# Kernel tuning notes

Measured on AMD Instinct MI355X. Metric: run time of the kernel, lower is better.

Reference implementation:

```python
import jax, jax.numpy as jnp
from jax import lax
import numpy as np

B, C, O, NF, H, W = 4, 64, 64, 64, 128, 128
DK = 3
K = DK * DK
PAD = DK // 2


def setup_inputs() -> dict:
    key = jax.random.key(0)
    k0, k1, k2, k3 = jax.random.split(key, 4)
    inputs = jax.random.normal(k0, (B, C, H, W), jnp.float32)
    feat = jax.random.normal(k1, (B, NF, H, W), jnp.float32)
    # small offset-conv weights keep learned offsets in a realistic sub-pixel range
    om_w = jax.random.normal(k2, (C * 3 * K, NF, 3, 3), jnp.float32) * 0.02
    om_b = jnp.zeros((C * 3 * K,), jnp.float32)
    dc_w = jax.random.normal(k3, (O, C, DK, DK), jnp.float32) * (1.0 / np.sqrt(C * K))
    dc_b = jnp.zeros((O,), jnp.float32)
    return dict(inputs=inputs, feat=feat, om_w=om_w, om_b=om_b, dc_w=dc_w, dc_b=dc_b)


def _gather(img, y, x):
    # img: [B,C,H,W]; y,x: int32 [B,C,K,H,W]; zero outside bounds
    valid = (y >= 0) & (y < H) & (x >= 0) & (x < W)
    yc = jnp.clip(y, 0, H - 1)
    xc = jnp.clip(x, 0, W - 1)
    idx = (yc * W + xc).reshape(B, C, K, H * W)
    flat = img.reshape(B, C, 1, H * W)
    v = jnp.take_along_axis(flat, idx, axis=3).reshape(B, C, K, H, W)
    return jnp.where(valid, v, 0.0)


def _forward(inputs, feat, om_w, om_b, dc_w, dc_b):
    # offset/mask conv: nf -> in_nc*3*K, 3x3, pad 1
    off_msk = lax.conv_general_dilated(
        feat, om_w, (1, 1), ((1, 1), (1, 1)),
        dimension_numbers=('NCHW', 'OIHW', 'NCHW')) + om_b[None, :, None, None]
    # offsets interleaved (y,x) per kernel tap per deformable group (= channel)
    off = off_msk[:, :C * 2 * K].reshape(B, C, K, 2, H, W)
    msk = jax.nn.sigmoid(off_msk[:, C * 2 * K:]).reshape(B, C, K, H, W)

    ky = (jnp.arange(K) // DK - PAD).astype(jnp.float32)  # [K]
    kx = (jnp.arange(K) % DK - PAD).astype(jnp.float32)
    hg = jnp.arange(H, dtype=jnp.float32)
    wg = jnp.arange(W, dtype=jnp.float32)
    py = hg[None, None, None, :, None] + ky[None, None, :, None, None] + off[:, :, :, 0]  # [B,C,K,H,W]
    px = wg[None, None, None, None, :] + kx[None, None, :, None, None] + off[:, :, :, 1]

    y0f = jnp.floor(py); x0f = jnp.floor(px)
    wy = py - y0f; wx = px - x0f
    y0 = y0f.astype(jnp.int32); x0 = x0f.astype(jnp.int32)
    y1 = y0 + 1; x1 = x0 + 1

    v00 = _gather(inputs, y0, x0)
    v01 = _gather(inputs, y0, x1)
    v10 = _gather(inputs, y1, x0)
    v11 = _gather(inputs, y1, x1)
    sampled = ((1 - wy) * (1 - wx) * v00 + (1 - wy) * wx * v01
               + wy * (1 - wx) * v10 + wy * wx * v11) * msk  # [B,C,K,H,W]

    out = jnp.einsum('bckhw,ock->bohw', sampled, dc_w.reshape(O, C, K))
    out = out + dc_b[None, :, None, None]
    return jax.nn.relu(out)


def reference(inputs, feat, om_w, om_b, dc_w, dc_b):
    return _forward(inputs, feat, om_w, om_b, dc_w, dc_b)
```

## Files before the change

### kernel.cpp

```cpp
#include <hip/hip_runtime.h>
#include <hip/hip_bf16.h>

typedef __bf16 bf16;
typedef __bf16 bf16x8 __attribute__((ext_vector_type(8)));
typedef __bf16 bf16x4 __attribute__((ext_vector_type(4)));
typedef float f32x4 __attribute__((ext_vector_type(4)));
typedef int i32x4 __attribute__((ext_vector_type(4)));

#define MFMA16(a, b, c) __builtin_amdgcn_mfma_f32_16x16x32_bf16((a), (b), (c), 0, 0, 0)

static constexpr size_t FEATS_OFF = 0;
static constexpr size_t OMW3_OFF  = 8388608;
static constexpr size_t OMB_OFF   = OMW3_OFF + 1990656;
static constexpr size_t DCW_OFF   = OMB_OFF + 6912;
static constexpr size_t PAD_OFF   = DCW_OFF + 73728;


__global__ void prep_featS(const float* __restrict__ feat, bf16* __restrict__ featS) {
    const int hh = blockIdx.x, b = blockIdx.y;
    __shared__ float t[64][129];
    for (int i = threadIdx.x; i < 64 * 32; i += 256) {
        int cf = i >> 5, q = i & 31;
        const float* src = feat + ((size_t)(b * 64 + cf) * 128 + hh) * 128 + q * 4;
        t[cf][q * 4 + 0] = src[0];
        t[cf][q * 4 + 1] = src[1];
        t[cf][q * 4 + 2] = src[2];
        t[cf][q * 4 + 3] = src[3];
    }
    __syncthreads();
    for (int i = threadIdx.x; i < 1024; i += 256) {
        int px = i >> 3, cfb = i & 7;
        int sb = cfb ^ (px & 7);
        bf16x8 v;
#pragma unroll
        for (int e = 0; e < 8; ++e) v[e] = (bf16)t[cfb * 8 + e][px];
        *(bf16x8*)(featS + ((size_t)((b * 128 + hh) * 128 + px) << 6) + sb * 8) = v;
    }
}

__global__ void prep_omw3(const float* __restrict__ om_w, bf16* __restrict__ out) {
    int i = blockIdx.x * 256 + threadIdx.x;
    if (i >= 995328) return;
    int e = i & 511, lane = e >> 3, j = e & 7;
    int q = i >> 9;
    int t = q % 3, q2 = q / 3, kk = q2 % 18, ct = q2 / 18;
    int ck = ct * 16 + (lane & 15);
    int kcol = kk * 32 + (lane >> 4) * 8 + j;
    int tap = kcol >> 6, cf = kcol & 63;
    int ch = (t < 2) ? (ck * 2 + t) : (1152 + ck);
    out[i] = (bf16)om_w[ch * 576 + cf * 9 + tap];
}

__global__ void prep_dcw2p(const float* __restrict__ dc_w, const float* __restrict__ om_b,
                           bf16* __restrict__ dcw2p, float* __restrict__ ombr) {
    int i = blockIdx.x * 256 + threadIdx.x;
    if (i < 36864) {
        int j = i & 7, lane = (i >> 3) & 63, ot = (i >> 9) & 3, win = i >> 11;
        int o = ot * 16 + (lane & 15);
        int ck = win * 32 + (lane >> 4) * 8 + j;
        dcw2p[i] = (bf16)dc_w[o * 576 + ck];
    }
    if (i < 1728) {
        int t = i / 576, ck = i - t * 576;
        int ch = (t < 2) ? (ck * 2 + t) : (1152 + ck);
        ombr[i] = om_b[ch];
    }
}

__global__ void prep_pad(const float* __restrict__ inputs, float* __restrict__ pad) {
    int yy = blockIdx.x, bc = blockIdx.y, xx = threadIdx.x;
    if (xx >= 134) return;
    float v = 0.f;
    if (yy >= 3 && yy <= 130 && xx >= 3 && xx <= 130)
        v = inputs[(size_t)bc * 16384 + (yy - 3) * 128 + (xx - 3)];
    pad[((size_t)bc * 134 + yy) * 134 + xx] = v;
}


__global__ void __launch_bounds__(256, 4)
deform_fused(const float* __restrict__ pad,
             const bf16* __restrict__ featS,
             const bf16* __restrict__ omw3,
             const float* __restrict__ ombr,
             const bf16* __restrict__ dcw2p,
             const float* __restrict__ dcb,
             float* __restrict__ out)
{
    const int bid = blockIdx.x;
    const int P0 = (bid & 1) << 6;
    const int h = (bid >> 1) & 127;
    const int b = bid >> 8;
    const int tid = threadIdx.x;
    const int lane = tid & 63, wid = tid >> 6;
    const int l15 = lane & 15, g = lane >> 4;

    __shared__ __align__(16) unsigned char smem[25344 + 8192];
    char* featB = (char*)smem;
    char* sampB = (char*)smem + 25344;

    for (int i = tid; i < 6336; i += 256) ((unsigned*)featB)[i] = 0u;
    __syncthreads();
    {
        const int s0 = (P0 == 0) ? 0 : 63;
        const int q0 = (P0 == 0) ? 1 : 0;
        for (int i = tid; i < 1560; i += 256) {
            int ky = i / 520, rem = i - ky * 520, row = rem >> 3, c = rem & 7;
            int hh = h - 1 + ky;
            if ((unsigned)hh < 128u) {
                const char* src = (const char*)featS
                    + (((size_t)(b * 128 + hh) * 128 + s0 + row) << 7) + c * 16;
                *(i32x4*)(featB + ((ky * 66 + q0 + row) << 7) + c * 16) = *(const i32x4*)src;
            }
        }
    }
    __syncthreads();

    f32x4 acc2[4];
#pragma unroll
    for (int u = 0; u < 4; ++u) acc2[u] = (f32x4){0.f, 0.f, 0.f, 0.f};

    const float* padb0 = pad + (size_t)b * 64 * 17956;
    const float fx0 = (float)(P0 + l15);

#pragma unroll 1
    for (int blk = 0; blk < 9; ++blk) {
        f32x4 acc1[3][4];
#pragma unroll
        for (int t = 0; t < 3; ++t)
#pragma unroll
            for (int nf = 0; nf < 4; ++nf) acc1[t][nf] = (f32x4){0.f, 0.f, 0.f, 0.f};

        const int ct = blk * 4 + wid;

#pragma unroll 2
        for (int kk = 0; kk < 18; ++kk) {
            const int tap = kk >> 1;
            const int kyp = tap / 3, kxp = tap - 3 * kyp;
            bf16x8 a0 = *(const bf16x8*)(omw3 + (size_t)(((ct * 18 + kk) * 3 + 0) * 512) + lane * 8);
            bf16x8 a1 = *(const bf16x8*)(omw3 + (size_t)(((ct * 18 + kk) * 3 + 1) * 512) + lane * 8);
            bf16x8 a2 = *(const bf16x8*)(omw3 + (size_t)(((ct * 18 + kk) * 3 + 2) * 512) + lane * 8);
            const int q = l15 + kxp;
            const int base = (kyp * 66 + q) * 128 + ((((kk & 1) * 4 + g) ^ ((q + 7) & 7)) << 4);
            bf16x8 bfr[4];
#pragma unroll
            for (int nf = 0; nf < 4; ++nf)
                bfr[nf] = *(const bf16x8*)(featB + base + nf * 2048);
            __builtin_amdgcn_s_setprio(1);
#pragma unroll
            for (int nf = 0; nf < 4; ++nf) {
                acc1[0][nf] = MFMA16(a0, bfr[nf], acc1[0][nf]);
                acc1[1][nf] = MFMA16(a1, bfr[nf], acc1[1][nf]);
                acc1[2][nf] = MFMA16(a2, bfr[nf], acc1[2][nf]);
            }
            __builtin_amdgcn_s_setprio(0);
        }

        bf16x8 aK0 = *(const bf16x8*)(dcw2p + (size_t)(((blk * 2 + 0) * 4 + wid) * 512) + lane * 8);
        bf16x8 aK1 = *(const bf16x8*)(dcw2p + (size_t)(((blk * 2 + 1) * 4 + wid) * 512) + lane * 8);

        {
            unsigned coff[4];
            float bye3[4], bxe3[4], bm[4];
#pragma unroll
            for (int r = 0; r < 4; ++r) {
                int ck = blk * 64 + wid * 16 + g * 4 + r;
                int c = ck / 9, kd = ck - 9 * c, kq = kd / 3;
                coff[r] = (unsigned)(c * 17956);
                bye3[r] = ombr[ck] + (float)(h + kq + 2);
                bxe3[r] = ombr[576 + ck] + (float)(kd - 3 * kq + 2);
                bm[r]   = ombr[1152 + ck];
            }
#pragma unroll
            for (int nf = 0; nf < 4; ++nf) {
                const float fxn = fx0 + 16.f * (float)nf;
                float s[4];
#pragma unroll
                for (int r = 0; r < 4; ++r) {
                    float py3 = acc1[0][nf][r] + bye3[r];
                    float px3 = acc1[1][nf][r] + bxe3[r] + fxn;
                    float lg  = acc1[2][nf][r] + bm[r];
                    py3 = fminf(fmaxf(py3, 0.5f), 132.5f);
                    px3 = fminf(fmaxf(px3, 0.5f), 132.5f);
                    int y03 = (int)py3, x03 = (int)px3;
                    float wy = py3 - (float)y03, wx = px3 - (float)x03;
                    unsigned uoff = coff[r] + (unsigned)(y03 * 134 + x03);
                    const float* p = padb0 + uoff;
                    float v00 = p[0], v01 = p[1], v10 = p[134], v11 = p[135];
                    float top = v00 + wx * (v01 - v00);
                    float bot = v10 + wx * (v11 - v10);
                    float bil = top + wy * (bot - top);
                    float msk = __builtin_amdgcn_rcpf(1.f + __expf(-lg));
                    s[r] = bil * msk;
                }
                bf16x4 pk = {(bf16)s[0], (bf16)s[1], (bf16)s[2], (bf16)s[3]};
                *(bf16x4*)(sampB + (nf * 16 + l15) * 128
                           + (((wid * 4 + g) ^ ((l15 & 7) << 1)) << 3)) = pk;
            }
        }
        __syncthreads();

        __builtin_amdgcn_s_setprio(1);
#pragma unroll
        for (int u = 0; u < 4; ++u) {
            const int rb = (u * 16 + l15) * 128;
            bf16x8 b0 = *(const bf16x8*)(sampB + rb + ((g ^ (l15 & 7)) << 4));
            bf16x8 b1 = *(const bf16x8*)(sampB + rb + (((4 + g) ^ (l15 & 7)) << 4));
            acc2[u] = MFMA16(aK0, b0, acc2[u]);
            acc2[u] = MFMA16(aK1, b1, acc2[u]);
        }
        __builtin_amdgcn_s_setprio(0);
        __syncthreads();
    }

    float bias[4];
#pragma unroll
    for (int r = 0; r < 4; ++r) bias[r] = dcb[wid * 16 + g * 4 + r];
#pragma unroll
    for (int u = 0; u < 4; ++u)
#pragma unroll
        for (int r = 0; r < 4; ++r) {
            int o = wid * 16 + g * 4 + r;
            out[((size_t)(b * 64 + o) * 128 + h) * 128 + P0 + u * 16 + l15]
                = fmaxf(acc2[u][r] + bias[r], 0.f);
        }
}

extern "C" void kernel_launch(void* const* d_in, const int* in_sizes, int n_in,
                              void* d_out, int out_size, void* d_ws, size_t ws_size,
                              hipStream_t stream) {
    const float* inputs = (const float*)d_in[0];
    const float* feat   = (const float*)d_in[1];
    const float* om_w   = (const float*)d_in[2];
    const float* om_b   = (const float*)d_in[3];
    const float* dc_w   = (const float*)d_in[4];
    const float* dc_b   = (const float*)d_in[5];
    float* out = (float*)d_out;

    char* ws = (char*)d_ws;
    bf16*  featS  = (bf16*)(ws + FEATS_OFF);
    bf16*  omw3   = (bf16*)(ws + OMW3_OFF);
    float* ombr   = (float*)(ws + OMB_OFF);
    bf16*  dcw2p  = (bf16*)(ws + DCW_OFF);
    float* pad    = (float*)(ws + PAD_OFF);

    prep_featS<<<dim3(128, 4), 256, 0, stream>>>(feat, featS);
    prep_omw3<<<(995328 + 255) / 256, 256, 0, stream>>>(om_w, omw3);
    prep_dcw2p<<<(36864 + 255) / 256, 256, 0, stream>>>(dc_w, om_b, dcw2p, ombr);
    prep_pad<<<dim3(134, 256), 256, 0, stream>>>(inputs, pad);

    deform_fused<<<1024, 256, 0, stream>>>(pad, featS, omw3, ombr, dcw2p, dc_b, out);
}
```

Measured before the change: 180.9 us.

## Merge weight prep kernels, precompute packed per-channel constants, streamline sampling address math

Merges the two weight-prep kernels into one launch. Precomputes per-channel bias plus tap-offset and channel-base constants into a packed f32x4 table, so the fused kernel loads them as vectors instead of doing divisions and scalar loads. The fused kernel also fully unrolls the 18-step offset-conv loop with precomputed LDS addresses, uses readfirstlane for the wave id, fmed3/fract intrinsics, and paired 2-float loads for the bilinear taps. These changes reduce launch count and integer/ALU overhead, at the cost of more registers from full unrolling and the fb array, which could lower occupancy.

```diff
diff --git a/kernel.cpp b/kernel.cpp
--- a/kernel.cpp
+++ b/kernel.cpp
@@ -5,15 +5,17 @@
 typedef __bf16 bf16x8 __attribute__((ext_vector_type(8)));
 typedef __bf16 bf16x4 __attribute__((ext_vector_type(4)));
 typedef float f32x4 __attribute__((ext_vector_type(4)));
-typedef int i32x4 __attribute__((ext_vector_type(4)));
+typedef float f32x2 __attribute__((ext_vector_type(2)));
+typedef float f32x2u __attribute__((ext_vector_type(2))) __attribute__((aligned(4)));
+typedef int  i32x4 __attribute__((ext_vector_type(4)));
 
 #define MFMA16(a, b, c) __builtin_amdgcn_mfma_f32_16x16x32_bf16((a), (b), (c), 0, 0, 0)
 
 static constexpr size_t FEATS_OFF = 0;
 static constexpr size_t OMW3_OFF  = 8388608;
-static constexpr size_t OMB_OFF   = OMW3_OFF + 1990656;
-static constexpr size_t DCW_OFF   = OMB_OFF + 6912;
-static constexpr size_t PAD_OFF   = DCW_OFF + 73728;
+static constexpr size_t DCW_OFF   = OMW3_OFF + 1990656;
+static constexpr size_t SC_OFF    = DCW_OFF + 73728;
+static constexpr size_t PAD_OFF   = SC_OFF + 9216;
 
 
 __global__ void prep_featS(const float* __restrict__ feat, bf16* __restrict__ featS) {
@@ -38,32 +40,35 @@
     }
 }
 
-__global__ void prep_omw3(const float* __restrict__ om_w, bf16* __restrict__ out) {
+__global__ void prep_weights(const float* __restrict__ om_w, const float* __restrict__ om_b,
+                             const float* __restrict__ dc_w,
+                             bf16* __restrict__ omw3, bf16* __restrict__ dcw2p,
+                             float* __restrict__ scf) {
     int i = blockIdx.x * 256 + threadIdx.x;
-    if (i >= 995328) return;
-    int e = i & 511, lane = e >> 3, j = e & 7;
-    int q = i >> 9;
-    int t = q % 3, q2 = q / 3, kk = q2 % 18, ct = q2 / 18;
-    int ck = ct * 16 + (lane & 15);
-    int kcol = kk * 32 + (lane >> 4) * 8 + j;
-    int tap = kcol >> 6, cf = kcol & 63;
-    int ch = (t < 2) ? (ck * 2 + t) : (1152 + ck);
-    out[i] = (bf16)om_w[ch * 576 + cf * 9 + tap];
-}
-
-__global__ void prep_dcw2p(const float* __restrict__ dc_w, const float* __restrict__ om_b,
-                           bf16* __restrict__ dcw2p, float* __restrict__ ombr) {
-    int i = blockIdx.x * 256 + threadIdx.x;
+    if (i < 995328) {
+        int e = i & 511, lane = e >> 3, j = e & 7;
+        int q = i >> 9;
+        int t = q % 3, q2 = q / 3, kk = q2 % 18, ct = q2 / 18;
+        int ck = ct * 16 + (lane & 15);
+        int kcol = kk * 32 + (lane >> 4) * 8 + j;
+        int tap = kcol >> 6, cf = kcol & 63;
+        int ch = (t < 2) ? (ck * 2 + t) : (1152 + ck);
+        omw3[i] = (bf16)om_w[ch * 576 + cf * 9 + tap];
+    }
     if (i < 36864) {
         int j = i & 7, lane = (i >> 3) & 63, ot = (i >> 9) & 3, win = i >> 11;
         int o = ot * 16 + (lane & 15);
         int ck = win * 32 + (lane >> 4) * 8 + j;
         dcw2p[i] = (bf16)dc_w[o * 576 + ck];
     }
-    if (i < 1728) {
-        int t = i / 576, ck = i - t * 576;
-        int ch = (t < 2) ? (ck * 2 + t) : (1152 + ck);
-        ombr[i] = om_b[ch];
+    if (i < 576) {
+        int ck = i;
+        int c = ck / 9, kd = ck - 9 * c, kq = kd / 3, kx = kd - 3 * kq;
+        int pr = ck >> 1, lo = ck & 1;
+        scf[pr * 8 + 0 + lo] = om_b[ck * 2]     + (float)(kq + 2);
+        scf[pr * 8 + 2 + lo] = om_b[ck * 2 + 1] + (float)(kx + 2);
+        scf[pr * 8 + 4 + lo] = om_b[1152 + ck];
+        scf[pr * 8 + 6 + lo] = __uint_as_float((unsigned)(c * 17956));
     }
 }
 
@@ -81,8 +86,8 @@
 deform_fused(const float* __restrict__ pad,
              const bf16* __restrict__ featS,
              const bf16* __restrict__ omw3,
-             const float* __restrict__ ombr,
              const bf16* __restrict__ dcw2p,
+             const f32x4* __restrict__ sconst,
              const float* __restrict__ dcb,
              float* __restrict__ out)
 {
@@ -91,7 +96,8 @@
     const int h = (bid >> 1) & 127;
     const int b = bid >> 8;
     const int tid = threadIdx.x;
-    const int lane = tid & 63, wid = tid >> 6;
+    const int lane = tid & 63;
+    const int wid_s = __builtin_amdgcn_readfirstlane(tid >> 6);
     const int l15 = lane & 15, g = lane >> 4;
 
     __shared__ __align__(16) unsigned char smem[25344 + 8192];
@@ -115,12 +121,25 @@
     }
     __syncthreads();
 
+    int fb[18];
+#pragma unroll
+    for (int kk = 0; kk < 18; ++kk) {
+        const int tap = kk >> 1;
+        const int kyp = tap / 3, kxp = tap - 3 * kyp;
+        const int q = l15 + kxp;
+        fb[kk] = (kyp * 66 + q) * 128 + ((((kk & 1) * 4 + g) ^ ((q + 7) & 7)) << 4);
+    }
+
     f32x4 acc2[4];
 #pragma unroll
     for (int u = 0; u < 4; ++u) acc2[u] = (f32x4){0.f, 0.f, 0.f, 0.f};
 
+    const bf16* omw3_l = omw3 + lane * 8;
+    const bf16* dcw_l  = dcw2p + lane * 8;
     const float* padb0 = pad + (size_t)b * 64 * 17956;
-    const float fx0 = (float)(P0 + l15);
+    const f32x2 hb2 = {(float)h, (float)h};
+    const f32x2 fx2 = {(float)(P0 + l15), (float)(P0 + l15)};
+    const int g4 = g * 4;
 
 #pragma unroll 1
     for (int blk = 0; blk < 9; ++blk) {
@@ -130,21 +149,17 @@
 #pragma unroll
             for (int nf = 0; nf < 4; ++nf) acc1[t][nf] = (f32x4){0.f, 0.f, 0.f, 0.f};
 
-        const int ct = blk * 4 + wid;
-
-#pragma unroll 2
+        const int abase = (blk * 4 + wid_s) * 27648;
+
+#pragma unroll
         for (int kk = 0; kk < 18; ++kk) {
-            const int tap = kk >> 1;
-            const int kyp = tap / 3, kxp = tap - 3 * kyp;
-            bf16x8 a0 = *(const bf16x8*)(omw3 + (size_t)(((ct * 18 + kk) * 3 + 0) * 512) + lane * 8);
-            bf16x8 a1 = *(const bf16x8*)(omw3 + (size_t)(((ct * 18 + kk) * 3 + 1) * 512) + lane * 8);
-            bf16x8 a2 = *(const bf16x8*)(omw3 + (size_t)(((ct * 18 + kk) * 3 + 2) * 512) + lane * 8);
-            const int q = l15 + kxp;
-            const int base = (kyp * 66 + q) * 128 + ((((kk & 1) * 4 + g) ^ ((q + 7) & 7)) << 4);
+            bf16x8 a0 = *(const bf16x8*)(omw3_l + abase + ((kk * 3 + 0) << 9));
+            bf16x8 a1 = *(const bf16x8*)(omw3_l + abase + ((kk * 3 + 1) << 9));
+            bf16x8 a2 = *(const bf16x8*)(omw3_l + abase + ((kk * 3 + 2) << 9));
             bf16x8 bfr[4];
 #pragma unroll
             for (int nf = 0; nf < 4; ++nf)
-                bfr[nf] = *(const bf16x8*)(featB + base + nf * 2048);
+                bfr[nf] = *(const bf16x8*)(featB + fb[kk] + nf * 2048);
             __builtin_amdgcn_s_setprio(1);
 #pragma unroll
             for (int nf = 0; nf < 4; ++nf) {
@@ -155,56 +170,62 @@
             __builtin_amdgcn_s_setprio(0);
         }
 
-        bf16x8 aK0 = *(const bf16x8*)(dcw2p + (size_t)(((blk * 2 + 0) * 4 + wid) * 512) + lane * 8);
-        bf16x8 aK1 = *(const bf16x8*)(dcw2p + (size_t)(((blk * 2 + 1) * 4 + wid) * 512) + lane * 8);
-
-        {
-            unsigned coff[4];
-            float bye3[4], bxe3[4], bm[4];
-#pragma unroll
-            for (int r = 0; r < 4; ++r) {
-                int ck = blk * 64 + wid * 16 + g * 4 + r;
-                int c = ck / 9, kd = ck - 9 * c, kq = kd / 3;
-                coff[r] = (unsigned)(c * 17956);
-                bye3[r] = ombr[ck] + (float)(h + kq + 2);
-                bxe3[r] = ombr[576 + ck] + (float)(kd - 3 * kq + 2);
-                bm[r]   = ombr[1152 + ck];
+        bf16x8 aK0 = *(const bf16x8*)(dcw_l + ((blk * 8 + wid_s) << 9));
+        bf16x8 aK1 = *(const bf16x8*)(dcw_l + ((blk * 8 + 4 + wid_s) << 9));
+
+        const f32x4* scB = sconst + (blk * 64 + wid_s * 16);
+        f32x4 e0A = scB[g4 + 0], e1A = scB[g4 + 1];
+        f32x4 e0B = scB[g4 + 2], e1B = scB[g4 + 3];
+        f32x2 yb[2], xb[2], mb[2];
+        unsigned co[2][2];
+        yb[0] = f32x2{e0A.x, e0A.y} + hb2;
+        xb[0] = f32x2{e0A.z, e0A.w} + fx2;
+        mb[0] = f32x2{e1A.x, e1A.y};
+        co[0][0] = __float_as_uint(e1A.z); co[0][1] = __float_as_uint(e1A.w);
+        yb[1] = f32x2{e0B.x, e0B.y} + hb2;
+        xb[1] = f32x2{e0B.z, e0B.w} + fx2;
+        mb[1] = f32x2{e1B.x, e1B.y};
+        co[1][0] = __float_as_uint(e1B.z); co[1][1] = __float_as_uint(e1B.w);
+
+#pragma unroll
+        for (int nf = 0; nf < 4; ++nf) {
+            float s[4];
+#pragma unroll
+            for (int pi = 0; pi < 2; ++pi) {
+                f32x2 py = f32x2{acc1[0][nf][2 * pi], acc1[0][nf][2 * pi + 1]} + yb[pi];
+                f32x2 px = f32x2{acc1[1][nf][2 * pi], acc1[1][nf][2 * pi + 1]} + xb[pi];
+                f32x2 lg = f32x2{acc1[2][nf][2 * pi], acc1[2][nf][2 * pi + 1]} + mb[pi];
+#pragma unroll
+                for (int e = 0; e < 2; ++e) {
+                    float pyc = __builtin_amdgcn_fmed3f(py[e], 0.5f, 132.5f);
+                    float pxc = __builtin_amdgcn_fmed3f(px[e], 0.5f, 132.5f);
+                    int y0 = (int)pyc, x0 = (int)pxc;
+                    float wy = __builtin_amdgcn_fractf(pyc);
+                    float wx = __builtin_amdgcn_fractf(pxc);
+                    unsigned off = co[pi][e] + (unsigned)(y0 * 134 + x0);
+                    f32x2u t0 = *(const f32x2u*)(padb0 + off);
+                    f32x2u t1 = *(const f32x2u*)(padb0 + off + 134);
+                    float top = t0.x + wx * (t0.y - t0.x);
+                    float bot = t1.x + wx * (t1.y - t1.x);
+                    float bil = top + wy * (bot - top);
+                    float mk = __builtin_amdgcn_rcpf(1.f + __expf(-lg[e]));
+                    s[2 * pi + e] = bil * mk;
+                }
             }
-#pragma unroll
-            for (int nf = 0; nf < 4; ++nf) {
-                const float fxn = fx0 + 16.f * (float)nf;
-                float s[4];
-#pragma unroll
-                for (int r = 0; r < 4; ++r) {
-                    float py3 = acc1[0][nf][r] + bye3[r];
-                    float px3 = acc1[1][nf][r] + bxe3[r] + fxn;
-                    float lg  = acc1[2][nf][r] + bm[r];
-                    py3 = fminf(fmaxf(py3, 0.5f), 132.5f);
-                    px3 = fminf(fmaxf(px3, 0.5f), 132.5f);
-                    int y03 = (int)py3, x03 = (int)px3;
-                    float wy = py3 - (float)y03, wx = px3 - (float)x03;
-                    unsigned uoff = coff[r] + (unsigned)(y03 * 134 + x03);
-                    const float* p = padb0 + uoff;
-                    float v00 = p[0], v01 = p[1], v10 = p[134], v11 = p[135];
-                    float top = v00 + wx * (v01 - v00);
-                    float bot = v10 + wx * (v11 - v10);
-                    float bil = top + wy * (bot - top);
-                    float msk = __builtin_amdgcn_rcpf(1.f + __expf(-lg));
-                    s[r] = bil * msk;
-                }
-                bf16x4 pk = {(bf16)s[0], (bf16)s[1], (bf16)s[2], (bf16)s[3]};
-                *(bf16x4*)(sampB + (nf * 16 + l15) * 128
-                           + (((wid * 4 + g) ^ ((l15 & 7) << 1)) << 3)) = pk;
-            }
+            bf16x4 pk4 = {(bf16)s[0], (bf16)s[1], (bf16)s[2], (bf16)s[3]};
+            *(bf16x4*)(sampB + (nf * 16 + l15) * 128
+                       + (((wid_s * 4 + g) ^ ((l15 & 7) << 1)) << 3)) = pk4;
+            xb[0] += 16.f; xb[1] += 16.f;
         }
         __syncthreads();
 
+        const int rb_swz = (g ^ (l15 & 7)) << 4;
         __builtin_amdgcn_s_setprio(1);
 #pragma unroll
         for (int u = 0; u < 4; ++u) {
-            const int rb = (u * 16 + l15) * 128;
-            bf16x8 b0 = *(const bf16x8*)(sampB + rb + ((g ^ (l15 & 7)) << 4));
-            bf16x8 b1 = *(const bf16x8*)(sampB + rb + (((4 + g) ^ (l15 & 7)) << 4));
+            const int rb = (u * 16 + l15) * 128 + rb_swz;
+            bf16x8 b0 = *(const bf16x8*)(sampB + rb);
+            bf16x8 b1 = *(const bf16x8*)(sampB + (rb ^ 64));
             acc2[u] = MFMA16(aK0, b0, acc2[u]);
             acc2[u] = MFMA16(aK1, b1, acc2[u]);
         }
@@ -214,12 +235,12 @@
 
     float bias[4];
 #pragma unroll
-    for (int r = 0; r < 4; ++r) bias[r] = dcb[wid * 16 + g * 4 + r];
+    for (int r = 0; r < 4; ++r) bias[r] = dcb[wid_s * 16 + g * 4 + r];
 #pragma unroll
     for (int u = 0; u < 4; ++u)
 #pragma unroll
         for (int r = 0; r < 4; ++r) {
-            int o = wid * 16 + g * 4 + r;
+            int o = wid_s * 16 + g * 4 + r;
             out[((size_t)(b * 64 + o) * 128 + h) * 128 + P0 + u * 16 + l15]
                 = fmaxf(acc2[u][r] + bias[r], 0.f);
         }
@@ -239,14 +260,14 @@
     char* ws = (char*)d_ws;
     bf16*  featS  = (bf16*)(ws + FEATS_OFF);
     bf16*  omw3   = (bf16*)(ws + OMW3_OFF);
-    float* ombr   = (float*)(ws + OMB_OFF);
     bf16*  dcw2p  = (bf16*)(ws + DCW_OFF);
+    float* scf    = (float*)(ws + SC_OFF);
     float* pad    = (float*)(ws + PAD_OFF);
 
     prep_featS<<<dim3(128, 4), 256, 0, stream>>>(feat, featS);
-    prep_omw3<<<(995328 + 255) / 256, 256, 0, stream>>>(om_w, omw3);
-    prep_dcw2p<<<(36864 + 255) / 256, 256, 0, stream>>>(dc_w, om_b, dcw2p, ombr);
+    prep_weights<<<(995328 + 255) / 256, 256, 0, stream>>>(om_w, om_b, dc_w, omw3, dcw2p, scf);
     prep_pad<<<dim3(134, 256), 256, 0, stream>>>(inputs, pad);
 
-    deform_fused<<<1024, 256, 0, stream>>>(pad, featS, omw3, ombr, dcw2p, dc_b, out);
-}
+    deform_fused<<<1024, 256, 0, stream>>>(pad, featS, omw3, dcw2p,
+                                           (const f32x4*)scf, dc_b, out);
+}
```

Result: faster. 177.2 us (-2.0%).
